# Performance work log

Hardware: AMD Instinct MI355X
Metric: run time of the kernel (lower is better)

## Reference

```python
import jax, jax.numpy as jnp
import numpy as np

N = 50000
E = 800000
IN_C = 128
HID_C = 64
OUT_C = 64
HEADS = 4
NEG_SLOPE = 0.2


def setup_inputs() -> dict:
    key = jax.random.key(0)
    ks = jax.random.split(key, 12)
    x = jax.random.normal(ks[0], (N, IN_C), dtype=jnp.float32)
    edge_index = jax.random.randint(ks[1], (2, E), 0, N, dtype=jnp.int32)
    s = 0.1
    # layer 1 params (GATConv: shared lin for src/dst, att vectors per head, bias over H*C)
    W1 = jax.random.normal(ks[2], (IN_C, HEADS * HID_C), dtype=jnp.float32) * s
    att_src1 = jax.random.normal(ks[3], (HEADS, HID_C), dtype=jnp.float32) * s
    att_dst1 = jax.random.normal(ks[4], (HEADS, HID_C), dtype=jnp.float32) * s
    b1 = jnp.zeros((HEADS * HID_C,), dtype=jnp.float32)
    # layer 2 params
    W2 = jax.random.normal(ks[5], (HEADS * HID_C, HEADS * OUT_C), dtype=jnp.float32) * s
    att_src2 = jax.random.normal(ks[6], (HEADS, OUT_C), dtype=jnp.float32) * s
    att_dst2 = jax.random.normal(ks[7], (HEADS, OUT_C), dtype=jnp.float32) * s
    b2 = jnp.zeros((HEADS * OUT_C,), dtype=jnp.float32)
    return {"x": x, "edge_index": edge_index,
            "W1": W1, "att_src1": att_src1, "att_dst1": att_dst1, "b1": b1,
            "W2": W2, "att_src2": att_src2, "att_dst2": att_dst2, "b2": b2}


def _segment_softmax(e, dst, n):
    # e: [E, H], softmax over edges sharing the same dst node, per head
    m = jax.ops.segment_max(e, dst, num_segments=n)        # [N, H]
    ex = jnp.exp(e - m[dst])
    z = jax.ops.segment_sum(ex, dst, num_segments=n)       # [N, H]
    return ex / (z[dst] + 1e-16)


def _gat_layer(x, src, dst, W, att_src, att_dst, bias, heads, out_c):
    n = x.shape[0]
    h = (x @ W).reshape(n, heads, out_c)                   # [N, H, C]
    a_s = jnp.einsum('nhc,hc->nh', h, att_src)             # [N, H]
    a_d = jnp.einsum('nhc,hc->nh', h, att_dst)
    e = jax.nn.leaky_relu(a_s[src] + a_d[dst], NEG_SLOPE)  # [E, H]
    alpha = _segment_softmax(e, dst, n)                    # [E, H]
    msg = alpha[:, :, None] * h[src]                       # [E, H, C]
    out = jax.ops.segment_sum(msg, dst, num_segments=n)    # [N, H, C]
    return out.reshape(n, heads * out_c) + bias


def reference(x, edge_index, W1, att_src1, att_dst1, b1, W2, att_src2, att_dst2, b2):
    # PyG GATConv adds self-loops by default
    loops = jnp.arange(N, dtype=edge_index.dtype)
    src = jnp.concatenate([edge_index[0], loops])
    dst = jnp.concatenate([edge_index[1], loops])
    h = jax.nn.elu(_gat_layer(x, src, dst, W1, att_src1, att_dst1, b1, HEADS, HID_C))
    out = jax.nn.elu(_gat_layer(h, src, dst, W2, att_src2, att_dst2, b2, HEADS, OUT_C))
    return out  # [N, HEADS*OUT_C]
```

## Files before the change

kernel.cpp:

```cpp
#include <hip/hip_runtime.h>
#include <hip/hip_fp16.h>
#include <math.h>


#define LEAKY_SLOPE 0.2f

typedef __attribute__((ext_vector_type(8))) short short8v;
typedef __attribute__((ext_vector_type(8))) _Float16 half8v;
typedef __attribute__((ext_vector_type(4))) float float4v;


__global__ void prep_kernel(const float* __restrict__ W1, __half* __restrict__ Bt1,
                            const float* __restrict__ W2, __half* __restrict__ Bt2,
                            const float* __restrict__ x, __half* __restrict__ x_h,
                            const int* __restrict__ ei, int* __restrict__ cnt,
                            int E, int N, int xblocks) {
    int b = blockIdx.x;
    if (b < 128) {
        int idx = b * 256 + threadIdx.x;
        int k = idx >> 8, c = idx & 255;
        Bt1[c * 128 + k] = __float2half(W1[idx]);
    } else if (b < 384) {
        int idx = (b - 128) * 256 + threadIdx.x;
        int k = idx >> 8, c = idx & 255;
        Bt2[c * 256 + k] = __float2half(W2[idx]);
    } else if (b < 384 + xblocks) {
        int t = (b - 384) * 256 + threadIdx.x;
        if (t < N * 32) {
            float4 v = *(const float4*)&x[(size_t)t * 4];
            __half2 h01 = __floats2half2_rn(v.x, v.y);
            __half2 h23 = __floats2half2_rn(v.z, v.w);
            uint2 pk = {*(unsigned*)&h01, *(unsigned*)&h23};
            *(uint2*)&x_h[(size_t)t * 4] = pk;
        }
    } else {
        int e = (b - 384 - xblocks) * 256 + threadIdx.x;
        if (e < E + N) {
            int dst = (e < E) ? ei[E + e] : (e - E);
            atomicAdd(&cnt[dst], 1);
        }
    }
}


__global__ __launch_bounds__(1024) void scan_block(const int* __restrict__ cnt,
                                                   int* __restrict__ row_start,
                                                   int* __restrict__ partials,
                                                   int n) {
    __shared__ int wsum[16];
    int tid = threadIdx.x, lane = tid & 63, wid = tid >> 6;
    int gi = blockIdx.x * 1024 + tid;
    int v = (gi < n) ? ((cnt[gi] + 1) & ~1) : 0;
    int x = v;
#pragma unroll
    for (int off = 1; off < 64; off <<= 1) {
        int y = __shfl_up(x, off, 64);
        if (lane >= off) x += y;
    }
    if (lane == 63) wsum[wid] = x;
    __syncthreads();
    if (wid == 0 && lane < 16) {
        int w = wsum[lane];
#pragma unroll
        for (int off = 1; off < 16; off <<= 1) {
            int y = __shfl_up(w, off, 16);
            if (lane >= off) w += y;
        }
        wsum[lane] = w;
    }
    __syncthreads();
    int excl = x - v + ((wid > 0) ? wsum[wid - 1] : 0);
    if (gi < n) row_start[gi] = excl;
    if (tid == 1023) partials[blockIdx.x] = wsum[15];
}

__global__ void scan_partials(int* __restrict__ partials, int nb) {
    int lane = threadIdx.x;
    int v = (lane < nb) ? partials[lane] : 0;
    int x = v;
#pragma unroll
    for (int off = 1; off < 64; off <<= 1) {
        int y = __shfl_up(x, off, 64);
        if (lane >= off) x += y;
    }
    if (lane < nb) partials[lane] = x - v;
    if (lane == nb - 1) partials[nb] = x;
}

__global__ __launch_bounds__(1024) void scan_add(int* __restrict__ row_start,
                                                 const int* __restrict__ partials,
                                                 int n, int nb) {
    int gi = blockIdx.x * 1024 + threadIdx.x;
    if (gi < n) row_start[gi] += partials[blockIdx.x];
    if (gi == 0) row_start[n] = partials[nb];
}

__global__ void scatter_kernel(const int* __restrict__ ei,
                               const int* __restrict__ row_start,
                               int* __restrict__ fill,
                               int2* __restrict__ edge_sd, int E, int Etot) {
    int e = blockIdx.x * blockDim.x + threadIdx.x;
    if (e >= Etot) return;
    int src, dst;
    if (e < E) { src = ei[e]; dst = ei[E + e]; }
    else       { src = e - E; dst = e - E; }
    int pos = row_start[dst] + atomicAdd(&fill[dst], 1);
    edge_sd[pos] = make_int2(src, dst);
}

__global__ void fill_rec(const int2* __restrict__ edge_sd,
                         const __half* __restrict__ a_s_h,
                         const float* __restrict__ a_d,
                         uint4* __restrict__ rec, int EtotMax) {
    int i = blockIdx.x * blockDim.x + threadIdx.x;
    if (i >= EtotMax) return;
    int2 sd = edge_sd[i];
    if (sd.x < 0) {
        uint4 z = {0u, 0u, 0u, 0u};
        rec[i] = z;
        return;
    }
    uint2 as2 = *(const uint2*)&a_s_h[(size_t)sd.x * 4];
    float4 ad4 = *(const float4*)&a_d[(size_t)sd.y * 4];
    float2 f01 = __half22float2(*(const __half2*)&as2.x);
    float2 f23 = __half22float2(*(const __half2*)&as2.y);
    float e0 = f01.x + ad4.x, e1 = f01.y + ad4.y;
    float e2 = f23.x + ad4.z, e3 = f23.y + ad4.w;
    e0 = (e0 > 0.f) ? e0 : LEAKY_SLOPE * e0;
    e1 = (e1 > 0.f) ? e1 : LEAKY_SLOPE * e1;
    e2 = (e2 > 0.f) ? e2 : LEAKY_SLOPE * e2;
    e3 = (e3 > 0.f) ? e3 : LEAKY_SLOPE * e3;
    __half2 w01 = __floats2half2_rn(__expf(e0), __expf(e1));
    __half2 w23 = __floats2half2_rn(__expf(e2), __expf(e3));
    uint4 r = {(unsigned)sd.x, *(unsigned*)&w01, *(unsigned*)&w23, 0u};
    rec[i] = r;
}


template <int K>
__global__ __launch_bounds__(256) void gemm_mfma(
    const __half* __restrict__ Ah, const __half* __restrict__ Bt,
    __half* __restrict__ Ch,
    const float* __restrict__ att_src, const float* __restrict__ att_dst,
    __half* __restrict__ a_s_out, float* __restrict__ a_d_out, int M) {
    __shared__ short As[128][40];
    __shared__ short Bs[128][40];

    const int col0 = (blockIdx.x & 1) * 128;
    const int row0 = (blockIdx.x >> 1) * 128;
    const int tid = threadIdx.x;
    const int lane = tid & 63;
    const int wave = tid >> 6;
    const int wr = wave >> 1, wc = wave & 1;
    const int quad = lane >> 4, lc = lane & 15;

    float4v acc[4][4] = {};

    const short* Abits = (const short*)Ah;
    const short* Bbits = (const short*)Bt;

    for (int k0 = 0; k0 < K; k0 += 32) {
#pragma unroll
        for (int i = 0; i < 2; i++) {
            int slot = tid + i * 256;
            int r = slot >> 2;
            int ko = (slot & 3) * 8;
            short8v v = {};
            int gr = row0 + r;
            if (gr < M) v = *(const short8v*)&Abits[(size_t)gr * K + k0 + ko];
            *(short8v*)&As[r][ko] = v;
        }
#pragma unroll
        for (int i = 0; i < 2; i++) {
            int slot = tid + i * 256;
            int r = slot >> 2;
            int ko = (slot & 3) * 8;
            short8v v = *(const short8v*)&Bbits[(size_t)(col0 + r) * K + k0 + ko];
            *(short8v*)&Bs[r][ko] = v;
        }
        __syncthreads();

        half8v a[4], bv[4];
#pragma unroll
        for (int mt = 0; mt < 4; mt++) {
            int r = wr * 64 + mt * 16 + lc;
            a[mt] = *(const half8v*)&As[r][quad * 8];
        }
#pragma unroll
        for (int nt = 0; nt < 4; nt++) {
            int n = wc * 64 + nt * 16 + lc;
            bv[nt] = *(const half8v*)&Bs[n][quad * 8];
        }
#pragma unroll
        for (int mt = 0; mt < 4; mt++)
#pragma unroll
            for (int nt = 0; nt < 4; nt++)
                acc[mt][nt] = __builtin_amdgcn_mfma_f32_16x16x32_f16(
                    a[mt], bv[nt], acc[mt][nt], 0, 0, 0);
        __syncthreads();
    }

    const int head = (col0 >> 6) + wc;
    float as_c[4], ad_c[4];
#pragma unroll
    for (int nt = 0; nt < 4; nt++) {
        as_c[nt] = att_src[head * 64 + nt * 16 + lc];
        ad_c[nt] = att_dst[head * 64 + nt * 16 + lc];
    }

#pragma unroll
    for (int mt = 0; mt < 4; mt++) {
#pragma unroll
        for (int r = 0; r < 4; r++) {
            int gr = row0 + wr * 64 + mt * 16 + quad * 4 + r;
            float ps = 0.f, pd = 0.f;
#pragma unroll
            for (int nt = 0; nt < 4; nt++) {
                float c = acc[mt][nt][r];
                ps = fmaf(c, as_c[nt], ps);
                pd = fmaf(c, ad_c[nt], pd);
                if (gr < M)
                    Ch[(size_t)gr * 256 + col0 + wc * 64 + nt * 16 + lc] =
                        __float2half(c);
            }
#pragma unroll
            for (int off = 1; off < 16; off <<= 1) {
                ps += __shfl_xor(ps, off, 64);
                pd += __shfl_xor(pd, off, 64);
            }
            if (lc == 0 && gr < M) {
                a_s_out[gr * 4 + head] = __float2half(ps);
                a_d_out[gr * 4 + head] = pd;
            }
        }
    }
}


template <bool OUT_HALF>
__global__ __launch_bounds__(256) void gat_aggregate(
    const __half* __restrict__ hh, const uint4* __restrict__ rec,
    const int* __restrict__ row_start, const float* __restrict__ bias,
    void* __restrict__ outp, int n) {
    int node = (blockIdx.x * blockDim.x + threadIdx.x) >> 6;
    if (node >= n) return;
    int lane = threadIdx.x & 63;
    int half = lane >> 5, l32 = lane & 31;
    int head = l32 >> 3;
    unsigned wsh = (head & 1) << 4;

    int beg = row_start[node];
    int end = row_start[node + 1];

    float l = 0.f;
    float acc[8] = {};

    uint4 r0 = rec[beg + half];
    uint4 r1 = rec[beg + 2 + half];
    uint4 r2 = rec[beg + 4 + half];
    uint4 r3 = rec[beg + 6 + half];

#define GATH(rr) (*(const uint4*)&hh[(size_t)(rr).x * 256 + l32 * 8])
#define PROC(rr, vv)                                                      \
    {                                                                     \
        unsigned u = (head & 2) ? (rr).z : (rr).y;                        \
        unsigned short us = (unsigned short)(u >> wsh);                   \
        float w = __half2float(*(const __half*)&us);                      \
        l += w;                                                           \
        const __half2* hp = (const __half2*)&(vv);                        \
        float2 f0 = __half22float2(hp[0]);                                \
        float2 f1 = __half22float2(hp[1]);                                \
        float2 f2 = __half22float2(hp[2]);                                \
        float2 f3 = __half22float2(hp[3]);                                \
        acc[0] = fmaf(w, f0.x, acc[0]); acc[1] = fmaf(w, f0.y, acc[1]);   \
        acc[2] = fmaf(w, f1.x, acc[2]); acc[3] = fmaf(w, f1.y, acc[3]);   \
        acc[4] = fmaf(w, f2.x, acc[4]); acc[5] = fmaf(w, f2.y, acc[5]);   \
        acc[6] = fmaf(w, f3.x, acc[6]); acc[7] = fmaf(w, f3.y, acc[7]);   \
    }

    uint4 h0 = GATH(r0);
    uint4 h1 = GATH(r1);
    uint4 h2 = GATH(r2);
    uint4 h3;

    int p = beg;
    while (p < end) {
        h3 = GATH(r3);
        PROC(r0, h0);
        r0 = rec[p + 8 + half];
        p += 2;
        if (p >= end) break;
        h0 = GATH(r0);
        PROC(r1, h1);
        r1 = rec[p + 8 + half];
        p += 2;
        if (p >= end) break;
        h1 = GATH(r1);
        PROC(r2, h2);
        r2 = rec[p + 8 + half];
        p += 2;
        if (p >= end) break;
        h2 = GATH(r2);
        PROC(r3, h3);
        r3 = rec[p + 8 + half];
        p += 2;
    }
#undef GATH
#undef PROC

    l += __shfl_xor(l, 32);
#pragma unroll
    for (int j = 0; j < 8; j++) acc[j] += __shfl_xor(acc[j], 32);

    if (half == 0) {
        float rcp = 1.f / l;
        float4 b0 = *(const float4*)&bias[l32 * 8];
        float4 b1 = *(const float4*)&bias[l32 * 8 + 4];
        float o[8];
        o[0] = fmaf(acc[0], rcp, b0.x); o[1] = fmaf(acc[1], rcp, b0.y);
        o[2] = fmaf(acc[2], rcp, b0.z); o[3] = fmaf(acc[3], rcp, b0.w);
        o[4] = fmaf(acc[4], rcp, b1.x); o[5] = fmaf(acc[5], rcp, b1.y);
        o[6] = fmaf(acc[6], rcp, b1.z); o[7] = fmaf(acc[7], rcp, b1.w);
#pragma unroll
        for (int j = 0; j < 8; j++)
            o[j] = (o[j] > 0.f) ? o[j] : __expf(o[j]) - 1.f;
        if constexpr (OUT_HALF) {
            __half2 q0 = __floats2half2_rn(o[0], o[1]);
            __half2 q1 = __floats2half2_rn(o[2], o[3]);
            __half2 q2 = __floats2half2_rn(o[4], o[5]);
            __half2 q3 = __floats2half2_rn(o[6], o[7]);
            uint4 pk = {*(unsigned*)&q0, *(unsigned*)&q1,
                        *(unsigned*)&q2, *(unsigned*)&q3};
            __half* outh = (__half*)outp;
            *(uint4*)&outh[(size_t)node * 256 + l32 * 8] = pk;
        } else {
            float* outf = (float*)outp;
            *(float4*)&outf[(size_t)node * 256 + l32 * 8] = *(float4*)&o[0];
            *(float4*)&outf[(size_t)node * 256 + l32 * 8 + 4] = *(float4*)&o[4];
        }
    }
}


extern "C" void kernel_launch(void* const* d_in, const int* in_sizes, int n_in,
                              void* d_out, int out_size, void* d_ws, size_t ws_size,
                              hipStream_t stream) {
    const float* x   = (const float*)d_in[0];
    const int*   ei  = (const int*)d_in[1];
    const float* W1  = (const float*)d_in[2];
    const float* as1 = (const float*)d_in[3];
    const float* ad1 = (const float*)d_in[4];
    const float* b1  = (const float*)d_in[5];
    const float* W2  = (const float*)d_in[6];
    const float* as2 = (const float*)d_in[7];
    const float* ad2 = (const float*)d_in[8];
    const float* b2  = (const float*)d_in[9];
    float* out = (float*)d_out;

    const int N = in_sizes[0] / 128;
    const int E = in_sizes[1] / 2;
    const int Etot = E + N;
    const int EtotMax = Etot + N + 8;
    const int NB = (N + 1023) / 1024;

    __half* h_half = (__half*)d_ws;
    __half* x1_h   = h_half + (size_t)N * 256;
    uint4*  rec    = (uint4*)(x1_h + (size_t)N * 256);
    __half* a_s_h  = (__half*)(rec + EtotMax);
    float*  a_d    = (float*)(a_s_h + (size_t)N * 4);
    __half* Bt1    = (__half*)(a_d + (size_t)N * 4);
    __half* Bt2    = Bt1 + 256 * 128;
    int*    cnt    = (int*)(Bt2 + 256 * 256);
    int*    fill   = cnt + N;
    int*    row_st = fill + N;
    int2*   edge_sd = (int2*)(row_st + (N + 2));
    int*    partials = (int*)(edge_sd + EtotMax);

    hipMemsetAsync(cnt, 0, sizeof(int) * 2 * (size_t)N, stream);
    hipMemsetAsync(edge_sd, 0xFF, sizeof(int2) * (size_t)EtotMax, stream);

    const int xblocks = (N * 32 + 255) / 256;
    const int eblocks = (Etot + 255) / 256;
    prep_kernel<<<384 + xblocks + eblocks, 256, 0, stream>>>(
        W1, Bt1, W2, Bt2, x, x1_h, ei, cnt, E, N, xblocks);

    scan_block<<<NB, 1024, 0, stream>>>(cnt, row_st, partials, N);
    scan_partials<<<1, 64, 0, stream>>>(partials, NB);
    scan_add<<<NB, 1024, 0, stream>>>(row_st, partials, N, NB);
    scatter_kernel<<<eblocks, 256, 0, stream>>>(ei, row_st, fill, edge_sd, E, Etot);

    dim3 ggrid(2 * ((N + 127) / 128));
    int ablocks = (N + 3) / 4;
    int fblocks = (EtotMax + 255) / 256;

    gemm_mfma<128><<<ggrid, 256, 0, stream>>>(x1_h, Bt1, h_half,
                                              as1, ad1, a_s_h, a_d, N);
    fill_rec<<<fblocks, 256, 0, stream>>>(edge_sd, a_s_h, a_d, rec, EtotMax);
    gat_aggregate<true><<<ablocks, 256, 0, stream>>>(h_half, rec, row_st,
                                                     b1, x1_h, N);
    gemm_mfma<256><<<ggrid, 256, 0, stream>>>(x1_h, Bt2, h_half,
                                              as2, ad2, a_s_h, a_d, N);
    fill_rec<<<fblocks, 256, 0, stream>>>(edge_sd, a_s_h, a_d, rec, EtotMax);
    gat_aggregate<false><<<ablocks, 256, 0, stream>>>(h_half, rec, row_st,
                                                      b2, out, N);
}
```

Measured before the change: 387.6 us.

## Fold partial scan into scan_add, pair edges in fill_rec, prefetch GEMM tiles

Removes the separate scan_partials launch by having every scan_add block redo the tiny 64-lane partial scan itself. fill_rec now handles two edges per thread through int4 loads, with EtotMax rounded to an even count. The MFMA GEMM prefetches the next K tile's global loads into registers while the current tile is computed, so memory latency overlaps the matrix math. In exchange it uses more registers in the GEMM, repeats the partial scan in every block, and depends on edge_sd being 16-byte aligned.

```diff
diff --git a/kernel.cpp b/kernel.cpp
--- a/kernel.cpp
+++ b/kernel.cpp
@@ -74,25 +74,26 @@
     if (tid == 1023) partials[blockIdx.x] = wsum[15];
 }
 
-__global__ void scan_partials(int* __restrict__ partials, int nb) {
-    int lane = threadIdx.x;
-    int v = (lane < nb) ? partials[lane] : 0;
-    int x = v;
-#pragma unroll
-    for (int off = 1; off < 64; off <<= 1) {
-        int y = __shfl_up(x, off, 64);
-        if (lane >= off) x += y;
-    }
-    if (lane < nb) partials[lane] = x - v;
-    if (lane == nb - 1) partials[nb] = x;
-}
-
 __global__ __launch_bounds__(1024) void scan_add(int* __restrict__ row_start,
                                                  const int* __restrict__ partials,
                                                  int n, int nb) {
+    __shared__ int spart[2];
+    if (threadIdx.x < 64) {
+        int lane = threadIdx.x;
+        int v = (lane < nb) ? partials[lane] : 0;
+        int x = v;
+#pragma unroll
+        for (int off = 1; off < 64; off <<= 1) {
+            int y = __shfl_up(x, off, 64);
+            if (lane >= off) x += y;
+        }
+        if (lane == (int)blockIdx.x) spart[0] = x - v;
+        if (lane == nb - 1) spart[1] = x;
+    }
+    __syncthreads();
     int gi = blockIdx.x * 1024 + threadIdx.x;
-    if (gi < n) row_start[gi] += partials[blockIdx.x];
-    if (gi == 0) row_start[n] = partials[nb];
+    if (gi < n) row_start[gi] += spart[0];
+    if (gi == 0) row_start[n] = spart[1];
 }
 
 __global__ void scatter_kernel(const int* __restrict__ ei,
@@ -108,20 +109,15 @@
     edge_sd[pos] = make_int2(src, dst);
 }
 
-__global__ void fill_rec(const int2* __restrict__ edge_sd,
-                         const __half* __restrict__ a_s_h,
-                         const float* __restrict__ a_d,
-                         uint4* __restrict__ rec, int EtotMax) {
-    int i = blockIdx.x * blockDim.x + threadIdx.x;
-    if (i >= EtotMax) return;
-    int2 sd = edge_sd[i];
-    if (sd.x < 0) {
+__device__ __forceinline__ uint4 make_rec(int src, int dst,
+                                          const __half* __restrict__ a_s_h,
+                                          const float* __restrict__ a_d) {
+    if (src < 0) {
         uint4 z = {0u, 0u, 0u, 0u};
-        rec[i] = z;
-        return;
-    }
-    uint2 as2 = *(const uint2*)&a_s_h[(size_t)sd.x * 4];
-    float4 ad4 = *(const float4*)&a_d[(size_t)sd.y * 4];
+        return z;
+    }
+    uint2 as2 = *(const uint2*)&a_s_h[(size_t)src * 4];
+    float4 ad4 = *(const float4*)&a_d[(size_t)dst * 4];
     float2 f01 = __half22float2(*(const __half2*)&as2.x);
     float2 f23 = __half22float2(*(const __half2*)&as2.y);
     float e0 = f01.x + ad4.x, e1 = f01.y + ad4.y;
@@ -132,8 +128,21 @@
     e3 = (e3 > 0.f) ? e3 : LEAKY_SLOPE * e3;
     __half2 w01 = __floats2half2_rn(__expf(e0), __expf(e1));
     __half2 w23 = __floats2half2_rn(__expf(e2), __expf(e3));
-    uint4 r = {(unsigned)sd.x, *(unsigned*)&w01, *(unsigned*)&w23, 0u};
-    rec[i] = r;
+    uint4 r = {(unsigned)src, *(unsigned*)&w01, *(unsigned*)&w23, 0u};
+    return r;
+}
+
+__global__ void fill_rec(const int4* __restrict__ edge_sd2,
+                         const __half* __restrict__ a_s_h,
+                         const float* __restrict__ a_d,
+                         uint4* __restrict__ rec, int npairs) {
+    int i = blockIdx.x * blockDim.x + threadIdx.x;
+    if (i >= npairs) return;
+    int4 sd = edge_sd2[i];
+    uint4 r0 = make_rec(sd.x, sd.y, a_s_h, a_d);
+    uint4 r1 = make_rec(sd.z, sd.w, a_s_h, a_d);
+    rec[2 * i] = r0;
+    rec[2 * i + 1] = r1;
 }
 
 
@@ -159,26 +168,33 @@
     const short* Abits = (const short*)Ah;
     const short* Bbits = (const short*)Bt;
 
+    const int sr = tid >> 2;
+    const int ko = (tid & 3) * 8;
+    const int ga0 = row0 + sr, ga1 = ga0 + 64;
+    const size_t gb0 = (size_t)(col0 + sr) * K + ko;
+    const size_t gb1 = (size_t)(col0 + sr + 64) * K + ko;
+
+    short8v pa0, pa1, pb0, pb1;
+#define LOADT(k0)                                                          \
+    {                                                                      \
+        pa0 = {}; pa1 = {};                                                \
+        if (ga0 < M) pa0 = *(const short8v*)&Abits[(size_t)ga0 * K + (k0) + ko]; \
+        if (ga1 < M) pa1 = *(const short8v*)&Abits[(size_t)ga1 * K + (k0) + ko]; \
+        pb0 = *(const short8v*)&Bbits[gb0 + (k0)];                         \
+        pb1 = *(const short8v*)&Bbits[gb1 + (k0)];                         \
+    }
+
+    LOADT(0);
+
+#pragma unroll
     for (int k0 = 0; k0 < K; k0 += 32) {
-#pragma unroll
-        for (int i = 0; i < 2; i++) {
-            int slot = tid + i * 256;
-            int r = slot >> 2;
-            int ko = (slot & 3) * 8;
-            short8v v = {};
-            int gr = row0 + r;
-            if (gr < M) v = *(const short8v*)&Abits[(size_t)gr * K + k0 + ko];
-            *(short8v*)&As[r][ko] = v;
-        }
-#pragma unroll
-        for (int i = 0; i < 2; i++) {
-            int slot = tid + i * 256;
-            int r = slot >> 2;
-            int ko = (slot & 3) * 8;
-            short8v v = *(const short8v*)&Bbits[(size_t)(col0 + r) * K + k0 + ko];
-            *(short8v*)&Bs[r][ko] = v;
-        }
+        *(short8v*)&As[sr][ko] = pa0;
+        *(short8v*)&As[sr + 64][ko] = pa1;
+        *(short8v*)&Bs[sr][ko] = pb0;
+        *(short8v*)&Bs[sr + 64][ko] = pb1;
         __syncthreads();
+
+        if (k0 + 32 < K) LOADT(k0 + 32);
 
         half8v a[4], bv[4];
 #pragma unroll
@@ -199,6 +215,7 @@
                     a[mt], bv[nt], acc[mt][nt], 0, 0, 0);
         __syncthreads();
     }
+#undef LOADT
 
     const int head = (col0 >> 6) + wc;
     float as_c[4], ad_c[4];
@@ -360,7 +377,7 @@
     const int N = in_sizes[0] / 128;
     const int E = in_sizes[1] / 2;
     const int Etot = E + N;
-    const int EtotMax = Etot + N + 8;
+    const int EtotMax = (Etot + N + 9) & ~1;
     const int NB = (N + 1023) / 1024;
 
     __half* h_half = (__half*)d_ws;
@@ -385,22 +402,24 @@
         W1, Bt1, W2, Bt2, x, x1_h, ei, cnt, E, N, xblocks);
 
     scan_block<<<NB, 1024, 0, stream>>>(cnt, row_st, partials, N);
-    scan_partials<<<1, 64, 0, stream>>>(partials, NB);
     scan_add<<<NB, 1024, 0, stream>>>(row_st, partials, N, NB);
     scatter_kernel<<<eblocks, 256, 0, stream>>>(ei, row_st, fill, edge_sd, E, Etot);
 
     dim3 ggrid(2 * ((N + 127) / 128));
     int ablocks = (N + 3) / 4;
-    int fblocks = (EtotMax + 255) / 256;
+    int npairs = EtotMax / 2;
+    int fblocks = (npairs + 255) / 256;
 
     gemm_mfma<128><<<ggrid, 256, 0, stream>>>(x1_h, Bt1, h_half,
                                               as1, ad1, a_s_h, a_d, N);
-    fill_rec<<<fblocks, 256, 0, stream>>>(edge_sd, a_s_h, a_d, rec, EtotMax);
+    fill_rec<<<fblocks, 256, 0, stream>>>((const int4*)edge_sd, a_s_h, a_d,
+                                          rec, npairs);
     gat_aggregate<true><<<ablocks, 256, 0, stream>>>(h_half, rec, row_st,
                                                      b1, x1_h, N);
     gemm_mfma<256><<<ggrid, 256, 0, stream>>>(x1_h, Bt2, h_half,
                                               as2, ad2, a_s_h, a_d, N);
-    fill_rec<<<fblocks, 256, 0, stream>>>(edge_sd, a_s_h, a_d, rec, EtotMax);
+    fill_rec<<<fblocks, 256, 0, stream>>>((const int4*)edge_sd, a_s_h, a_d,
+                                          rec, npairs);
     gat_aggregate<false><<<ablocks, 256, 0, stream>>>(h_half, rec, row_st,
                                                       b2, out, N);
 }
```

Result: no change. 380.6 us (-1.8%).
